# Optimization experiments

Measured on AMD Instinct MI355X. Metric: run time of the kernel, lower is better.

Reference implementation:

```python
import jax, jax.numpy as jnp
import numpy as np

N_NODES = 100000
N_EDGES = 3200000
D_IN = 256
D_OUT = 256


def setup_inputs() -> dict:
    key = jax.random.key(0)
    k1, k2, k3, k4, k5, k6 = jax.random.split(key, 6)
    x = jax.random.normal(k1, (N_NODES, D_IN), dtype=jnp.float32)
    edge_src = jax.random.randint(k2, (N_EDGES,), 0, N_NODES, dtype=jnp.int32)
    edge_dst = jax.random.randint(k3, (N_EDGES,), 0, N_NODES, dtype=jnp.int32)
    edge_weight = jax.random.uniform(k4, (N_EDGES,), dtype=jnp.float32)
    weight = jax.random.normal(k5, (D_IN, D_OUT), dtype=jnp.float32) * 0.02
    bias = jax.random.uniform(k6, (D_OUT,), dtype=jnp.float32)
    return {"x": x, "edge_src": edge_src, "edge_dst": edge_dst,
            "edge_weight": edge_weight, "weight": weight, "bias": bias}


def reference(x, edge_src, edge_dst, edge_weight, weight, bias):
    # support = X @ W  (dense GEMM)
    support = x @ weight  # [N, D_OUT]
    # output = A @ support, A given as COO edges (dst <- src with weight)
    msgs = support[edge_src] * edge_weight[:, None]  # [E, D_OUT]
    out = jax.ops.segment_sum(msgs, edge_dst, num_segments=N_NODES)  # [N, D_OUT]
    return out + bias
```

## Files before the change

### kernel.cpp

```cpp
#include <hip/hip_runtime.h>
#include <hip/hip_bf16.h>

#define N_NODES 100000
#define N_EDGES 3200000
#define DDIM    256
#define M_PAD   100096
#define NBKT    782
#define BCAP    4608
#define EPB_A   4096
#define GCAP    2432

#define PREP_CONVW_BASE 782
#define PREP_CONVX_BASE 1038
#define PREP_GRID       13538

typedef __attribute__((ext_vector_type(8))) short short8;
typedef __attribute__((ext_vector_type(4))) float f32x4;

typedef const __attribute__((address_space(1))) void gvoid_t;
typedef __attribute__((address_space(3))) void lvoid_t;

__device__ __forceinline__ void load_lds16(const void* g, void* l) {
  __builtin_amdgcn_global_load_lds((gvoid_t*)g, (lvoid_t*)l, 16, 0, 0);
}

__device__ __forceinline__ unsigned short f2bf(float f) {
  __hip_bfloat16 h = __float2bfloat16(f);
  return *(unsigned short*)&h;
}
__device__ __forceinline__ float bflo(unsigned u) { return __uint_as_float(u << 16); }
__device__ __forceinline__ float bfhi(unsigned u) { return __uint_as_float(u & 0xffff0000u); }

__global__ __launch_bounds__(256) void prep_kernel(
    const float* __restrict__ x,  unsigned short* __restrict__ xb,
    const float* __restrict__ w,  unsigned short* __restrict__ wt,
    const int* __restrict__ src, const int* __restrict__ dst,
    const float* __restrict__ wgt,
    int* __restrict__ gcur, unsigned long long* __restrict__ region) {
  __shared__ unsigned long long staged[EPB_A];
  __shared__ unsigned short sbkt[EPB_A];
  __shared__ int lhist[NBKT];
  __shared__ int lstart[NBKT];
  __shared__ int lcur[NBKT];
  __shared__ int gb[NBKT];
  __shared__ int csum[256];

  const int bid = blockIdx.x;
  const int t = threadIdx.x;

  if (bid >= PREP_CONVX_BASE) {
    size_t i = (size_t)(bid - PREP_CONVX_BASE) * 256 + t;
    size_t idx = i * 8;
    float4 va = *(const float4*)(x + idx);
    float4 vb = *(const float4*)(x + idx + 4);
    short8 o;
    o[0] = (short)f2bf(va.x); o[1] = (short)f2bf(va.y);
    o[2] = (short)f2bf(va.z); o[3] = (short)f2bf(va.w);
    o[4] = (short)f2bf(vb.x); o[5] = (short)f2bf(vb.y);
    o[6] = (short)f2bf(vb.z); o[7] = (short)f2bf(vb.w);
    *(short8*)(xb + idx) = o;
    return;
  }
  if (bid >= PREP_CONVW_BASE) {
    int t2 = (bid - PREP_CONVW_BASE) * 256 + t;
    int n = t2 >> 8, k = t2 & 255;
    wt[t2] = f2bf(w[k * 256 + n]);
    return;
  }

  const int e0 = bid * EPB_A;
  const int ecnt = min(EPB_A, N_EDGES - e0);

  for (int i = t; i < NBKT; i += 256) lhist[i] = 0;
  __syncthreads();
  for (int k = t; k < ecnt; k += 256)
    atomicAdd(&lhist[dst[e0 + k] >> 7], 1);
  __syncthreads();

  int i0 = 4 * t;
  int a0 = (i0 + 0 < NBKT) ? lhist[i0 + 0] : 0;
  int a1 = (i0 + 1 < NBKT) ? lhist[i0 + 1] : 0;
  int a2 = (i0 + 2 < NBKT) ? lhist[i0 + 2] : 0;
  int a3 = (i0 + 3 < NBKT) ? lhist[i0 + 3] : 0;
  int s = a0 + a1 + a2 + a3;
  csum[t] = s;
  __syncthreads();
  for (int off = 1; off < 256; off <<= 1) {
    int v = (t >= off) ? csum[t - off] : 0;
    __syncthreads();
    csum[t] += v;
    __syncthreads();
  }
  int base = csum[t] - s;
  if (i0 + 0 < NBKT) lstart[i0 + 0] = base; base += a0;
  if (i0 + 1 < NBKT) lstart[i0 + 1] = base; base += a1;
  if (i0 + 2 < NBKT) lstart[i0 + 2] = base; base += a2;
  if (i0 + 3 < NBKT) lstart[i0 + 3] = base;
  __syncthreads();

  for (int i = t; i < NBKT; i += 256) {
    int c = lhist[i];
    int off = c ? atomicAdd(&gcur[i], c) : 0;
    gb[i] = i * BCAP + off;
    lcur[i] = lstart[i];
  }
  __syncthreads();

  for (int k = t; k < ecnt; k += 256) {
    int d  = dst[e0 + k];
    int sr = src[e0 + k];
    float wv = wgt[e0 + k];
    int b = d >> 7;
    int p = atomicAdd(&lcur[b], 1);
    staged[p] = ((unsigned long long)__float_as_uint(wv) << 32) |
                ((unsigned)(d & 127) << 17) | (unsigned)sr;
    sbkt[p] = (unsigned short)b;
  }
  __syncthreads();

  for (int j = t; j < ecnt; j += 256) {
    int b = sbkt[j];
    int addr = gb[b] + (j - lstart[b]);
    if (addr < (b + 1) * BCAP) region[addr] = staged[j];
  }
}

__global__ __launch_bounds__(256) void gemm_kernel(const unsigned short* __restrict__ xb,
                                                   const unsigned short* __restrict__ wt,
                                                   unsigned short* __restrict__ sup) {
  __shared__ unsigned short As[128 * 32];
  __shared__ unsigned short Bs[128 * 32];
  const int tid  = threadIdx.x;
  const int w    = tid >> 6;
  const int lane = tid & 63;
  const int quad = lane >> 4;
  const int l15  = lane & 15;
  const int wr   = w >> 1, wc = w & 1;
  const int m0 = blockIdx.x * 128;
  const int n0 = blockIdx.y * 128;

  f32x4 acc[4][4] = {};

  const int srow   = lane >> 2;
  const int schunk = (lane & 3) * 8;

  for (int kt = 0; kt < 256; kt += 32) {
#pragma unroll
    for (int i = 0; i < 2; ++i) {
      int r = w * 32 + i * 16 + srow;
      load_lds16(xb + ((size_t)(m0 + r) * 256 + kt + schunk),
                 As + (w * 32 + i * 16) * 32);
      load_lds16(wt + ((size_t)(n0 + r) * 256 + kt + schunk),
                 Bs + (w * 32 + i * 16) * 32);
    }
    __syncthreads();

    short8 a[4], b[4];
#pragma unroll
    for (int mi = 0; mi < 4; ++mi)
      a[mi] = *(const short8*)(As + (wr * 64 + mi * 16 + l15) * 32 + quad * 8);
#pragma unroll
    for (int ni = 0; ni < 4; ++ni)
      b[ni] = *(const short8*)(Bs + (wc * 64 + ni * 16 + l15) * 32 + quad * 8);

#pragma unroll
    for (int mi = 0; mi < 4; ++mi)
#pragma unroll
      for (int ni = 0; ni < 4; ++ni)
        acc[mi][ni] = __builtin_amdgcn_mfma_f32_16x16x32_bf16(a[mi], b[ni], acc[mi][ni], 0, 0, 0);
    __syncthreads();
  }

#pragma unroll
  for (int mi = 0; mi < 4; ++mi) {
#pragma unroll
    for (int r = 0; r < 4; ++r) {
      size_t row = (size_t)(m0 + wr * 64 + mi * 16 + quad * 4 + r);
#pragma unroll
      for (int ni = 0; ni < 4; ++ni) {
        int col = n0 + wc * 64 + ni * 16 + l15;
        sup[row * 256 + col] = f2bf(acc[mi][ni][r]);
      }
    }
  }
}

__global__ __launch_bounds__(256) void csr_gather_kernel(
    const unsigned long long* __restrict__ region,
    const int* __restrict__ gcur,
    const unsigned short* __restrict__ sup,
    const float* __restrict__ bias,
    float* __restrict__ out) {
  __shared__ unsigned long long lcsr[GCAP];
  __shared__ int lhist[64], loff[64], lcur[64];
  const int t = threadIdx.x;
  const int b = blockIdx.x;
  const int h = blockIdx.y;
  const int cnt = min(gcur[b], BCAP);
  const int base = b * BCAP;

  if (t < 64) lhist[t] = 0;
  __syncthreads();
  for (int j = t; j < cnt; j += 256) {
    unsigned lo = (unsigned)(region[base + j] & 0xffffffffu);
    int dl = (int)((lo >> 17) & 127);
    if ((dl >> 6) == h) atomicAdd(&lhist[dl & 63], 1);
  }
  __syncthreads();
  if (t < 64) loff[t] = lhist[t];
  __syncthreads();
  for (int off = 1; off < 64; off <<= 1) {
    int v = (t >= off && t < 64) ? loff[t - off] : 0;
    __syncthreads();
    if (t < 64) loff[t] += v;
    __syncthreads();
  }
  if (t < 64) { loff[t] -= lhist[t]; lcur[t] = loff[t]; }
  __syncthreads();
  for (int j = t; j < cnt; j += 256) {
    unsigned long long e = region[base + j];
    int dl = (int)((e >> 17) & 127);
    if ((dl >> 6) == h) {
      int p = atomicAdd(&lcur[dl & 63], 1);
      if (p < GCAP) lcsr[p] = e;
    }
  }
  __syncthreads();

  const int wv = t >> 6;
  const int c0 = (t & 63) * 4;
  float4 bv = *(const float4*)(bias + c0);

  for (int dl = wv; dl < 64; dl += 4) {
    int node = b * 128 + h * 64 + dl;
    if (node >= N_NODES) continue;
    int start = loff[dl];
    int end   = min(lcur[dl], GCAP);
    float a0 = bv.x, a1 = bv.y, a2 = bv.z, a3 = bv.w;

    int i = start;
    for (; i + 2 <= end; i += 2) {
      unsigned long long m0 = lcsr[i];
      unsigned long long m1 = lcsr[i + 1];
      int   s0 = (int)(m0 & 0x1ffffu);
      float w0 = __uint_as_float((unsigned)(m0 >> 32));
      int   s1 = (int)(m1 & 0x1ffffu);
      float w1 = __uint_as_float((unsigned)(m1 >> 32));
      uint2 p0 = *(const uint2*)(sup + (size_t)s0 * 256 + c0);
      uint2 p1 = *(const uint2*)(sup + (size_t)s1 * 256 + c0);
      a0 = fmaf(w0, bflo(p0.x), a0);
      a1 = fmaf(w0, bfhi(p0.x), a1);
      a2 = fmaf(w0, bflo(p0.y), a2);
      a3 = fmaf(w0, bfhi(p0.y), a3);
      a0 = fmaf(w1, bflo(p1.x), a0);
      a1 = fmaf(w1, bfhi(p1.x), a1);
      a2 = fmaf(w1, bflo(p1.y), a2);
      a3 = fmaf(w1, bfhi(p1.y), a3);
    }
    if (i < end) {
      unsigned long long m0 = lcsr[i];
      int   s0 = (int)(m0 & 0x1ffffu);
      float w0 = __uint_as_float((unsigned)(m0 >> 32));
      uint2 p0 = *(const uint2*)(sup + (size_t)s0 * 256 + c0);
      a0 = fmaf(w0, bflo(p0.x), a0);
      a1 = fmaf(w0, bfhi(p0.x), a1);
      a2 = fmaf(w0, bflo(p0.y), a2);
      a3 = fmaf(w0, bfhi(p0.y), a3);
    }
    *(float4*)(out + (size_t)node * 256 + c0) = make_float4(a0, a1, a2, a3);
  }
}

extern "C" void kernel_launch(void* const* d_in, const int* in_sizes, int n_in,
                              void* d_out, int out_size, void* d_ws, size_t ws_size,
                              hipStream_t stream) {
  const float* x        = (const float*)d_in[0];
  const int*   edge_src = (const int*)d_in[1];
  const int*   edge_dst = (const int*)d_in[2];
  const float* edge_w   = (const float*)d_in[3];
  const float* weight   = (const float*)d_in[4];
  const float* bias     = (const float*)d_in[5];
  float* out = (float*)d_out;

  char* ws = (char*)d_ws;
  size_t off = 0;
  auto alloc = [&](size_t bytes) -> void* {
    void* p = ws + off;
    off = (off + bytes + 255) & ~(size_t)255;
    return p;
  };

  unsigned short* wt  = (unsigned short*)alloc(256 * 256 * 2);
  unsigned short* sup = (unsigned short*)alloc((size_t)M_PAD * 256 * 2);
  unsigned long long* region = (unsigned long long*)alloc((size_t)NBKT * BCAP * 8);
  int* gcur = (int*)alloc(NBKT * 4);

  unsigned short* xb = (unsigned short*)d_out;

  hipMemsetAsync(gcur, 0, NBKT * 4, stream);
  prep_kernel<<<PREP_GRID, 256, 0, stream>>>(x, xb, weight, wt,
                                             edge_src, edge_dst, edge_w,
                                             gcur, region);
  gemm_kernel<<<dim3(782, 2), 256, 0, stream>>>(xb, wt, sup);
  csr_gather_kernel<<<dim3(NBKT, 2), 256, 0, stream>>>(region, gcur, sup, bias, out);
}
```

Measured before the change: 507.3 us.

## Fuse x bf16 conversion into GEMM and co-schedule GEMM with edge binning

Removes the separate x-to-bf16 pass and its xb buffer by converting fp32 x to bf16 inside the GEMM tile load. It merges the GEMM blocks and the edge-binning blocks into one launch with a shared LDS union, and halves edges per binning block. The gcur memset moves into the weight-conversion kernel. Each GEMM tile now reads fp32 x from global memory with plain loads instead of async LDS loads, and x is loaded twice because of the two N tiles.

```diff
diff --git a/kernel.cpp b/kernel.cpp
--- a/kernel.cpp
+++ b/kernel.cpp
@@ -7,12 +7,10 @@
 #define M_PAD   100096
 #define NBKT    782
 #define BCAP    4608
-#define EPB_A   4096
+#define EPB     2048
+#define NB_BINA 1563
+#define NB_GEMM 1564
 #define GCAP    2432
-
-#define PREP_CONVW_BASE 782
-#define PREP_CONVX_BASE 1038
-#define PREP_GRID       13538
 
 typedef __attribute__((ext_vector_type(8))) short short8;
 typedef __attribute__((ext_vector_type(4))) float f32x4;
@@ -31,45 +29,100 @@
 __device__ __forceinline__ float bflo(unsigned u) { return __uint_as_float(u << 16); }
 __device__ __forceinline__ float bfhi(unsigned u) { return __uint_as_float(u & 0xffff0000u); }
 
-__global__ __launch_bounds__(256) void prep_kernel(
-    const float* __restrict__ x,  unsigned short* __restrict__ xb,
-    const float* __restrict__ w,  unsigned short* __restrict__ wt,
+__global__ void convw_kernel(const float* __restrict__ w, unsigned short* __restrict__ wt,
+                             int* __restrict__ gcur) {
+  int t = blockIdx.x * blockDim.x + threadIdx.x;
+  int n = t >> 8, k = t & 255;
+  wt[t] = f2bf(w[k * 256 + n]);
+  if (t < NBKT) gcur[t] = 0;
+}
+
+__global__ __launch_bounds__(256) void gemm_binA_kernel(
+    const float* __restrict__ x, const unsigned short* __restrict__ wt,
+    unsigned short* __restrict__ sup,
     const int* __restrict__ src, const int* __restrict__ dst,
     const float* __restrict__ wgt,
     int* __restrict__ gcur, unsigned long long* __restrict__ region) {
-  __shared__ unsigned long long staged[EPB_A];
-  __shared__ unsigned short sbkt[EPB_A];
-  __shared__ int lhist[NBKT];
-  __shared__ int lstart[NBKT];
-  __shared__ int lcur[NBKT];
-  __shared__ int gb[NBKT];
-  __shared__ int csum[256];
-
+  __shared__ __align__(16) char smem[34816];
   const int bid = blockIdx.x;
   const int t = threadIdx.x;
 
-  if (bid >= PREP_CONVX_BASE) {
-    size_t i = (size_t)(bid - PREP_CONVX_BASE) * 256 + t;
-    size_t idx = i * 8;
-    float4 va = *(const float4*)(x + idx);
-    float4 vb = *(const float4*)(x + idx + 4);
-    short8 o;
-    o[0] = (short)f2bf(va.x); o[1] = (short)f2bf(va.y);
-    o[2] = (short)f2bf(va.z); o[3] = (short)f2bf(va.w);
-    o[4] = (short)f2bf(vb.x); o[5] = (short)f2bf(vb.y);
-    o[6] = (short)f2bf(vb.z); o[7] = (short)f2bf(vb.w);
-    *(short8*)(xb + idx) = o;
+  if (bid >= NB_BINA) {
+    unsigned short* As = (unsigned short*)smem;
+    unsigned short* Bs = (unsigned short*)(smem + 8192);
+    const int g  = bid - NB_BINA;
+    const int m0 = (g >> 1) * 128;
+    const int n0 = (g & 1) * 128;
+    const int w    = t >> 6;
+    const int lane = t & 63;
+    const int quad = lane >> 4;
+    const int l15  = lane & 15;
+    const int wr   = w >> 1, wc = w & 1;
+    const int srow   = lane >> 2;
+    const int schunk = (lane & 3) * 8;
+
+    f32x4 acc[4][4] = {};
+
+    for (int kt = 0; kt < 256; kt += 32) {
+#pragma unroll
+      for (int j = 0; j < 4; ++j) {
+        int f = j * 256 + t;
+        int row = f >> 3, c4 = (f & 7) * 4;
+        int xr = m0 + row; if (xr >= N_NODES) xr = N_NODES - 1;
+        float4 v = *(const float4*)(x + (size_t)xr * 256 + kt + c4);
+        ushort4 o;
+        o.x = f2bf(v.x); o.y = f2bf(v.y); o.z = f2bf(v.z); o.w = f2bf(v.w);
+        *(ushort4*)(As + row * 32 + c4) = o;
+      }
+#pragma unroll
+      for (int i = 0; i < 2; ++i) {
+        int r = w * 32 + i * 16 + srow;
+        load_lds16(wt + ((size_t)(n0 + r) * 256 + kt + schunk),
+                   Bs + (w * 32 + i * 16) * 32);
+      }
+      __syncthreads();
+
+      short8 a[4], b[4];
+#pragma unroll
+      for (int mi = 0; mi < 4; ++mi)
+        a[mi] = *(const short8*)(As + (wr * 64 + mi * 16 + l15) * 32 + quad * 8);
+#pragma unroll
+      for (int ni = 0; ni < 4; ++ni)
+        b[ni] = *(const short8*)(Bs + (wc * 64 + ni * 16 + l15) * 32 + quad * 8);
+
+#pragma unroll
+      for (int mi = 0; mi < 4; ++mi)
+#pragma unroll
+        for (int ni = 0; ni < 4; ++ni)
+          acc[mi][ni] = __builtin_amdgcn_mfma_f32_16x16x32_bf16(a[mi], b[ni], acc[mi][ni], 0, 0, 0);
+      __syncthreads();
+    }
+
+#pragma unroll
+    for (int mi = 0; mi < 4; ++mi) {
+#pragma unroll
+      for (int r = 0; r < 4; ++r) {
+        size_t row = (size_t)(m0 + wr * 64 + mi * 16 + quad * 4 + r);
+#pragma unroll
+        for (int ni = 0; ni < 4; ++ni) {
+          int col = n0 + wc * 64 + ni * 16 + l15;
+          sup[row * 256 + col] = f2bf(acc[mi][ni][r]);
+        }
+      }
+    }
     return;
   }
-  if (bid >= PREP_CONVW_BASE) {
-    int t2 = (bid - PREP_CONVW_BASE) * 256 + t;
-    int n = t2 >> 8, k = t2 & 255;
-    wt[t2] = f2bf(w[k * 256 + n]);
-    return;
-  }
-
-  const int e0 = bid * EPB_A;
-  const int ecnt = min(EPB_A, N_EDGES - e0);
+
+  unsigned long long* staged = (unsigned long long*)smem;
+  unsigned short* sbkt = (unsigned short*)(smem + 16384);
+  int* lhist  = (int*)(smem + 20480);
+  int* lstart = (int*)(smem + 23608);
+  int* lcur   = (int*)(smem + 26736);
+  int* gb     = (int*)(smem + 29864);
+  int* csum   = (int*)(smem + 32992);
+
+  const int e0 = bid * EPB;
+  const int ecnt = min(EPB, N_EDGES - e0);
 
   for (int i = t; i < NBKT; i += 256) lhist[i] = 0;
   __syncthreads();
@@ -122,66 +175,6 @@
     int b = sbkt[j];
     int addr = gb[b] + (j - lstart[b]);
     if (addr < (b + 1) * BCAP) region[addr] = staged[j];
-  }
-}
-
-__global__ __launch_bounds__(256) void gemm_kernel(const unsigned short* __restrict__ xb,
-                                                   const unsigned short* __restrict__ wt,
-                                                   unsigned short* __restrict__ sup) {
-  __shared__ unsigned short As[128 * 32];
-  __shared__ unsigned short Bs[128 * 32];
-  const int tid  = threadIdx.x;
-  const int w    = tid >> 6;
-  const int lane = tid & 63;
-  const int quad = lane >> 4;
-  const int l15  = lane & 15;
-  const int wr   = w >> 1, wc = w & 1;
-  const int m0 = blockIdx.x * 128;
-  const int n0 = blockIdx.y * 128;
-
-  f32x4 acc[4][4] = {};
-
-  const int srow   = lane >> 2;
-  const int schunk = (lane & 3) * 8;
-
-  for (int kt = 0; kt < 256; kt += 32) {
-#pragma unroll
-    for (int i = 0; i < 2; ++i) {
-      int r = w * 32 + i * 16 + srow;
-      load_lds16(xb + ((size_t)(m0 + r) * 256 + kt + schunk),
-                 As + (w * 32 + i * 16) * 32);
-      load_lds16(wt + ((size_t)(n0 + r) * 256 + kt + schunk),
-                 Bs + (w * 32 + i * 16) * 32);
-    }
-    __syncthreads();
-
-    short8 a[4], b[4];
-#pragma unroll
-    for (int mi = 0; mi < 4; ++mi)
-      a[mi] = *(const short8*)(As + (wr * 64 + mi * 16 + l15) * 32 + quad * 8);
-#pragma unroll
-    for (int ni = 0; ni < 4; ++ni)
-      b[ni] = *(const short8*)(Bs + (wc * 64 + ni * 16 + l15) * 32 + quad * 8);
-
-#pragma unroll
-    for (int mi = 0; mi < 4; ++mi)
-#pragma unroll
-      for (int ni = 0; ni < 4; ++ni)
-        acc[mi][ni] = __builtin_amdgcn_mfma_f32_16x16x32_bf16(a[mi], b[ni], acc[mi][ni], 0, 0, 0);
-    __syncthreads();
-  }
-
-#pragma unroll
-  for (int mi = 0; mi < 4; ++mi) {
-#pragma unroll
-    for (int r = 0; r < 4; ++r) {
-      size_t row = (size_t)(m0 + wr * 64 + mi * 16 + quad * 4 + r);
-#pragma unroll
-      for (int ni = 0; ni < 4; ++ni) {
-        int col = n0 + wc * 64 + ni * 16 + l15;
-        sup[row * 256 + col] = f2bf(acc[mi][ni][r]);
-      }
-    }
   }
 }
 
@@ -295,12 +288,9 @@
   unsigned long long* region = (unsigned long long*)alloc((size_t)NBKT * BCAP * 8);
   int* gcur = (int*)alloc(NBKT * 4);
 
-  unsigned short* xb = (unsigned short*)d_out;
-
-  hipMemsetAsync(gcur, 0, NBKT * 4, stream);
-  prep_kernel<<<PREP_GRID, 256, 0, stream>>>(x, xb, weight, wt,
-                                             edge_src, edge_dst, edge_w,
-                                             gcur, region);
-  gemm_kernel<<<dim3(782, 2), 256, 0, stream>>>(xb, wt, sup);
+  convw_kernel<<<256, 256, 0, stream>>>(weight, wt, gcur);
+  gemm_binA_kernel<<<NB_BINA + NB_GEMM, 256, 0, stream>>>(x, wt, sup,
+                                                          edge_src, edge_dst, edge_w,
+                                                          gcur, region);
   csr_gather_kernel<<<dim3(NBKT, 2), 256, 0, stream>>>(region, gcur, sup, bias, out);
 }
```

Result: no change. 504.1 us (-0.6%).
